# Kernel tuning notes

Measured on AMD Instinct MI355X. Metric: run time of the kernel, lower is better.

## Reference

```python
import jax, jax.numpy as jnp
import numpy as np

N_E = 512; KEY_DIM = 512; E_DIM = 512; E_SPLIT = 8
KT = 0.1; COE_EMA = 0.5; RATE = 1.2
HALF_PI = float(np.pi / 2.0)


def l2n(x, eps=1e-12):
    # torch F.normalize(p=2, dim=-1)
    return x / jnp.maximum(jnp.linalg.norm(x, axis=-1, keepdims=True), eps)


def sphere_emb(feature, t):
    # TimeSphereEncoder: lift unit feature in R^d to R^{d+1} with time angle
    # a = t * (pi/2) / rate ; out = [feature*cos(a), sin(a)]
    a = t * (HALF_PI / RATE)
    return jnp.concatenate([feature * jnp.cos(a)[..., None], jnp.sin(a)[..., None]], axis=-1)


def split_t_f(x):
    # inverse of sphere_emb for unit-norm x: recover (t, sin_component, feature)
    s = x[..., -1]
    t = jnp.arcsin(jnp.clip(s, -1.0, 1.0)) / (HALF_PI / RATE)
    f = l2n(x[..., :-1])
    return t, s, f


def split_norm(v):
    # split_vparams_norm: L2-normalize each of E_SPLIT contiguous chunks
    shp = v.shape
    d = E_DIM // E_SPLIT
    return l2n(v.reshape(shp[:-1] + (E_SPLIT, d))).reshape(shp)


def setup_inputs() -> dict:
    key = jax.random.key(0)
    k = jax.random.split(key, 6)
    key_soft = jax.random.normal(k[0], (32, 1024, KEY_DIM), jnp.float32)
    u_t = jax.random.uniform(k[1], (32, 1024), jnp.float32)
    keys_weight = l2n(jax.random.uniform(k[2], (N_E, KEY_DIM), jnp.float32, -1.0 / N_E, 1.0 / N_E))
    t_keys_weight = (jnp.arange(N_E, dtype=jnp.float32)[:, None]
                     + jax.random.uniform(k[3], (N_E, 1), jnp.float32)) / N_E
    r_keys_weight = jnp.full((N_E, 1), 0.999, jnp.float32)
    vparams_weight = jax.random.uniform(k[4], (N_E, E_DIM), jnp.float32, -1.0 / N_E, 1.0 / N_E)
    return {"key_soft": key_soft, "u_t": u_t, "keys_weight": keys_weight,
            "t_keys_weight": t_keys_weight, "r_keys_weight": r_keys_weight,
            "vparams_weight": vparams_weight}


def _forward(key_soft, u_t, keys_weight, t_keys_weight, r_keys_weight, vparams_weight):
    sg = jax.lax.stop_gradient
    B, T, D = key_soft.shape
    BT = B * T
    # normalize + time-embed tokens
    ks_emb = sphere_emb(l2n(key_soft), u_t)                       # (B,T,D+1)
    ks_flat = ks_emb.reshape(BT, D + 1)
    # codebook keys: normalized, time-embedded, detached, scaled by hardtanh(r)
    keys_norm = sphere_emb(l2n(keys_weight), t_keys_weight[:, 0])  # (n_e,D+1)
    r = jnp.clip(r_keys_weight, 0.0, 1.0)                          # (n_e,1)
    keysA = sg(keys_norm) * r
    score0 = ks_flat @ keysA.T                                     # (BT,n_e)
    idx0 = jnp.argmax(score0, axis=1)
    # --- EMA codebook update (all no-grad) ---
    ks_sg = sg(ks_flat)
    seg = jax.ops.segment_sum(ks_sg, idx0, num_segments=N_E)       # (n_e,D+1)
    cnt = jax.ops.segment_sum(jnp.ones((BT,), ks_sg.dtype), idx0, num_segments=N_E)[:, None]
    mean_ks = jnp.nan_to_num(seg / (1.0 + cnt))
    keys_new_full = l2n(sg(keysA) * COE_EMA + mean_ks * (1.0 - COE_EMA))
    t_new, _, feat_new = split_t_f(keys_new_full)
    index_switch = jnp.argsort(t_new)
    t_sorted = t_new[index_switch]
    keys_feat2 = feat_new[index_switch]
    r2 = jnp.clip(r_keys_weight[index_switch], 0.0, 1.0)
    vparams2 = vparams_weight[index_switch]
    idx1 = index_switch[idx0]
    cnt2 = jax.ops.segment_sum(jnp.ones((BT,), ks_sg.dtype), idx1, num_segments=N_E) + 1.0
    w_cnt = sg(jnp.nan_to_num(1.0 / cnt2)[idx1].reshape(B, T))
    # --- second scoring with updated codebook ---
    keys_norm2 = sphere_emb(l2n(keys_feat2), t_sorted)             # (n_e,D+1)
    keysB = sg(keys_norm2) * r2
    score = ks_flat @ keysB.T                                      # (BT,n_e)
    w = jnp.nan_to_num(jax.nn.softmax(score / KT, axis=-1))
    w_max = jnp.take_along_axis(w, idx1[:, None], axis=-1)[:, 0].reshape(B, T)
    vpn = split_norm(vparams2)
    vp_w = split_norm(w @ sg(vpn))                                 # (BT,e_dim)
    key_w = l2n(w @ sg(keysB))                                     # (BT,D+1)
    vparams_hard = split_norm(vparams2[idx1])
    key_hard_raw = keysB[idx1]
    vparams_hard = vp_w + sg(vparams_hard - vp_w)                  # straight-through
    key_hard = key_w + sg(key_hard_raw - key_w)
    return (idx1.reshape(B, T),
            key_hard.reshape(B, T, D + 1),
            vp_w.reshape(B, T, E_DIM),
            vparams_hard.reshape(B, T, E_DIM),
            w_max, w_cnt, ks_emb)


def reference(key_soft, u_t, keys_weight, t_keys_weight, r_keys_weight, vparams_weight):
    return _forward(key_soft, u_t, keys_weight, t_keys_weight, r_keys_weight, vparams_weight)
```

## Files before the change

kernel.cpp:

```cpp
#include <hip/hip_runtime.h>
#include <math.h>

constexpr int BT  = 32768;
constexpr int D   = 512;
constexpr int D1  = 513;
constexpr int NE  = 512;
constexpr int EDIM = 512;
constexpr int NCH = 128;
constexpr int SUB = 32;
constexpr int P1S = 520;
constexpr int AKP = 544;
constexpr int A16S = 2 * AKP;
#define KA 1.3089969389957472f

typedef _Float16 h16;
typedef _Float16 f16x8 __attribute__((ext_vector_type(8)));
typedef _Float16 f16x4 __attribute__((ext_vector_type(4)));
typedef float f32x4 __attribute__((ext_vector_type(4)));

__device__ __forceinline__ float wave_sum(float v) {
#pragma unroll
  for (int off = 32; off; off >>= 1) v += __shfl_xor(v, off);
  return v;
}

__global__ __launch_bounds__(256) void k_embed(const float* __restrict__ ks,
                                               const float* __restrict__ ut,
                                               float* __restrict__ emb) {
  int token = blockIdx.x * 4 + (threadIdx.x >> 6);
  int lane = threadIdx.x & 63;
  const float4* row4 = (const float4*)(ks + (size_t)token * D);
  float4 va = row4[lane * 2];
  float4 vb = row4[lane * 2 + 1];
  float ss = va.x * va.x + va.y * va.y + va.z * va.z + va.w * va.w
           + vb.x * vb.x + vb.y * vb.y + vb.z * vb.z + vb.w * vb.w;
  ss = wave_sum(ss);
  float inv = 1.0f / fmaxf(sqrtf(ss), 1e-12f);
  float a = ut[token] * KA;
  float c = cosf(a), s = sinf(a);
  float ic = inv * c;
  float* o = emb + (size_t)token * D1 + lane * 8;
  o[0] = va.x * ic; o[1] = va.y * ic; o[2] = va.z * ic; o[3] = va.w * ic;
  o[4] = vb.x * ic; o[5] = vb.y * ic; o[6] = vb.z * ic; o[7] = vb.w * ic;
  if (lane == 0) emb[(size_t)token * D1 + D] = s;
}

__global__ __launch_bounds__(64) void k_keysA(const float* __restrict__ kw,
                                              const float* __restrict__ tk,
                                              const float* __restrict__ rk,
                                              float* __restrict__ keysA,
                                              h16* __restrict__ BA) {
  int e = blockIdx.x; int lane = threadIdx.x;
  const float* row = kw + (size_t)e * D;
  float v[8]; float ss = 0.f;
#pragma unroll
  for (int i = 0; i < 8; i++) { v[i] = row[lane + 64 * i]; ss += v[i] * v[i]; }
  ss = wave_sum(ss);
  float inv = 1.0f / fmaxf(sqrtf(ss), 1e-12f);
  float a = tk[e] * KA;
  float r = fminf(fmaxf(rk[e], 0.f), 1.f);
  float c = cosf(a) * r, s = sinf(a) * r;
  float* o = keysA + (size_t)e * D1;
  h16* br = BA + (size_t)e * A16S;
#pragma unroll
  for (int i = 0; i < 8; i++) {
    float val = v[i] * inv * c;
    o[lane + 64 * i] = val;
    float x = val * 8.0f;
    h16 h = (h16)x;
    br[lane + 64 * i] = h;
    br[AKP + lane + 64 * i] = (h16)(x - (float)h);
  }
  if (lane == 0) {
    o[D] = s;
    float x = s * 8.0f;
    h16 h = (h16)x;
    br[512] = h;
    br[AKP + 512] = (h16)(x - (float)h);
  }
  if (lane >= 1 && lane < 32) {
    br[512 + lane] = (h16)0.f;
    br[AKP + 512 + lane] = (h16)0.f;
  }
}

template <int KP, int EPI, int ASRC, int TERMS>
__global__ __launch_bounds__(256) void k_gemm(const float* __restrict__ Af,
                                              const h16* __restrict__ Ai,
                                              const h16* __restrict__ Bp,
                                              float* __restrict__ C,
                                              unsigned short* __restrict__ W,
                                              float* __restrict__ pv,
                                              int* __restrict__ pi_,
                                              float* __restrict__ ps) {
  constexpr int NS = KP / 32;
  constexpr int LST = 36;
  __shared__ h16 Ah[128 * LST];
  __shared__ h16 Al[(TERMS >= 2) ? 128 * LST : 1];
  __shared__ h16 Bh[128 * LST];
  __shared__ h16 Bl[(TERMS >= 3) ? 128 * LST : 1];
  const int tid = threadIdx.x;
  const int bid = blockIdx.x;
  const int wg = (bid & 7) * (gridDim.x >> 3) + (bid >> 3);
  const int m0 = (wg >> 2) * 128;
  const int n0 = (wg & 3) * 128;
  const int nblk = wg & 3;
  const int lane = tid & 63;
  const int wid = tid >> 6;
  const int wr = wid >> 1, wc = wid & 1;
  const int l15 = lane & 15, l4 = lane >> 4;
  const int aB = (wr * 64 + l15) * LST + l4 * 8;
  const int bB = (wc * 64 + l15) * LST + l4 * 8;

  f32x4 acc[4][4] = {};

  auto loadAf = [&](int s, float fv[4][4]) {
    int k0 = s * 32;
    bool guard = (KP == AKP) && (k0 + 32 > D1);
#pragma unroll
    for (int p = 0; p < 4; ++p) {
      int row = (tid >> 3) + 32 * p;
      int fq = tid & 7;
      const float* ap = Af + (size_t)(m0 + row) * D1 + k0 + fq * 4;
      if (!guard) {
#pragma unroll
        for (int j = 0; j < 4; ++j) fv[p][j] = ap[j];
      } else {
#pragma unroll
        for (int j = 0; j < 4; ++j) {
          int c = k0 + fq * 4 + j;
          fv[p][j] = (c < D1) ? ap[j] : 0.f;
        }
      }
    }
  };
  auto writeAf = [&](float fv[4][4]) {
#pragma unroll
    for (int p = 0; p < 4; ++p) {
      int row = (tid >> 3) + 32 * p;
      int fq = tid & 7;
      f16x4 hh, ll;
#pragma unroll
      for (int j = 0; j < 4; ++j) {
        float x = fv[p][j] * 8.0f;
        h16 h = (h16)x;
        hh[j] = h;
        ll[j] = (h16)(x - (float)h);
      }
      *(f16x4*)&Ah[row * LST + fq * 4] = hh;
      if constexpr (TERMS >= 2) *(f16x4*)&Al[row * LST + fq * 4] = ll;
    }
  };
  auto loadAp = [&](int s, uint4 av[2]) {
    int k0 = s * 32;
#pragma unroll
    for (int p = 0; p < 2; ++p) {
      int lin = tid + 256 * p;
      int row = lin >> 2, q = lin & 3;
      av[p] = *(const uint4*)(Ai + (size_t)(m0 + row) * 512 + k0 + q * 8);
    }
  };
  auto writeAp = [&](uint4 av[2]) {
#pragma unroll
    for (int p = 0; p < 2; ++p) {
      int lin = tid + 256 * p;
      int row = lin >> 2, q = lin & 3;
      *(uint4*)&Ah[row * LST + q * 8] = av[p];
    }
  };
  constexpr int BPASS = (TERMS >= 3) ? 4 : 2;
  auto loadB = [&](int s, uint4 bv[BPASS]) {
    int k0 = s * 32;
#pragma unroll
    for (int p = 0; p < BPASS; ++p) {
      int lin = tid + 256 * p;
      int row = (lin >> 2) & 127;
      int half = lin >> 9;
      int q = lin & 3;
      bv[p] = *(const uint4*)(Bp + (size_t)(n0 + row) * (2 * KP) + half * KP + k0 + q * 8);
    }
  };
  auto writeB = [&](uint4 bv[BPASS]) {
#pragma unroll
    for (int p = 0; p < BPASS; ++p) {
      int lin = tid + 256 * p;
      int row = (lin >> 2) & 127;
      int half = lin >> 9;
      int q = lin & 3;
      h16* dst = (half && TERMS >= 3) ? Bl : Bh;
      *(uint4*)&dst[row * LST + q * 8] = bv[p];
    }
  };

  {
    uint4 bv[BPASS];
    loadB(0, bv);
    if constexpr (ASRC == 0) { float fv[4][4]; loadAf(0, fv); writeAf(fv); }
    else { uint4 av[2]; loadAp(0, av); writeAp(av); }
    writeB(bv);
  }
  __syncthreads();

  for (int s = 0; s < NS; ++s) {
    uint4 apn[2], bvn[BPASS]; float fvn[4][4];
    if (s + 1 < NS) {
      if constexpr (ASRC == 0) loadAf(s + 1, fvn);
      else loadAp(s + 1, apn);
      loadB(s + 1, bvn);
    }
    f16x8 ah[4], al_[4], bh_[4], bl_[4];
#pragma unroll
    for (int i = 0; i < 4; ++i) {
      ah[i] = *(const f16x8*)&Ah[aB + i * 16 * LST];
      if constexpr (TERMS >= 2) al_[i] = *(const f16x8*)&Al[aB + i * 16 * LST];
    }
#pragma unroll
    for (int j = 0; j < 4; ++j) {
      bh_[j] = *(const f16x8*)&Bh[bB + j * 16 * LST];
      if constexpr (TERMS >= 3) bl_[j] = *(const f16x8*)&Bl[bB + j * 16 * LST];
    }
    __syncthreads();
    if (s + 1 < NS) {
      if constexpr (ASRC == 0) writeAf(fvn);
      else writeAp(apn);
      writeB(bvn);
    }
#pragma unroll
    for (int j = 0; j < 4; ++j) {
#pragma unroll
      for (int i = 0; i < 4; ++i) {
        acc[i][j] = __builtin_amdgcn_mfma_f32_16x16x32_f16(ah[i], bh_[j], acc[i][j], 0, 0, 0);
        if constexpr (TERMS >= 2)
          acc[i][j] = __builtin_amdgcn_mfma_f32_16x16x32_f16(al_[i], bh_[j], acc[i][j], 0, 0, 0);
        if constexpr (TERMS >= 3)
          acc[i][j] = __builtin_amdgcn_mfma_f32_16x16x32_f16(ah[i], bl_[j], acc[i][j], 0, 0, 0);
      }
    }
    __syncthreads();
  }

  if constexpr (EPI == 1) {
#pragma unroll
    for (int i = 0; i < 4; ++i)
#pragma unroll
      for (int r = 0; r < 4; ++r) {
        float ss = 0.f;
#pragma unroll
        for (int j = 0; j < 4; ++j) ss += acc[i][j][r] * acc[i][j][r];
        ss += __shfl_xor(ss, 1); ss += __shfl_xor(ss, 2);
        ss += __shfl_xor(ss, 4); ss += __shfl_xor(ss, 8);
        float inv = 1.0f / fmaxf(sqrtf(ss), 1e-12f);
        int row = m0 + wr * 64 + i * 16 + l4 * 4 + r;
        float* cp = C + (size_t)row * 512 + n0 + wc * 64 + l15;
#pragma unroll
        for (int j = 0; j < 4; ++j) cp[j * 16] = acc[i][j][r] * inv;
      }
  } else if constexpr (EPI == 2) {
    float* lv = (float*)Ah;
    int*   li = (int*)Bh;
#pragma unroll
    for (int i = 0; i < 4; ++i)
#pragma unroll
      for (int r = 0; r < 4; ++r) {
        float bv = -INFINITY; int bidx = 0x7fffffff;
#pragma unroll
        for (int j = 0; j < 4; ++j) {
          float val = acc[i][j][r] * 0.015625f;
          int col = n0 + wc * 64 + j * 16 + l15;
          if (val > bv || (val == bv && col < bidx)) { bv = val; bidx = col; }
        }
#pragma unroll
        for (int off = 1; off < 16; off <<= 1) {
          float ov = __shfl_xor(bv, off);
          int oi = __shfl_xor(bidx, off);
          if (ov > bv || (ov == bv && oi < bidx)) { bv = ov; bidx = oi; }
        }
        if (l15 == 0) {
          int lr = wr * 64 + i * 16 + l4 * 4 + r;
          lv[wc * 128 + lr] = bv; li[wc * 128 + lr] = bidx;
        }
      }
    __syncthreads();
    if (tid < 128) {
      float v0 = lv[tid], v1 = lv[128 + tid];
      int i0 = li[tid], i1 = li[128 + tid];
      bool sec = (v1 > v0) || (v1 == v0 && i1 < i0);
      int row = m0 + tid;
      pv[(size_t)row * 4 + nblk] = sec ? v1 : v0;
      pi_[(size_t)row * 4 + nblk] = sec ? i1 : i0;
    }
  } else if constexpr (EPI == 3) {
    float* psW = (float*)Bh;
#pragma unroll
    for (int i = 0; i < 4; ++i)
#pragma unroll
      for (int r = 0; r < 4; ++r) {
        int row = m0 + wr * 64 + i * 16 + l4 * 4 + r;
        unsigned short* wp = W + (size_t)row * 512 + n0 + wc * 64 + l15;
        float se = 0.f;
#pragma unroll
        for (int j = 0; j < 4; ++j) {
          float v = acc[i][j][r] * 0.015625f;
          float w = __expf(10.f * v);
          se += w;
          h16 hh = (h16)w;
          wp[j * 16] = *(unsigned short*)&hh;
        }
        se += __shfl_xor(se, 1); se += __shfl_xor(se, 2);
        se += __shfl_xor(se, 4); se += __shfl_xor(se, 8);
        if (l15 == 0) psW[wc * 128 + wr * 64 + i * 16 + l4 * 4 + r] = se;
      }
    __syncthreads();
    if (tid < 128)
      ps[(size_t)(m0 + tid) * 4 + nblk] = psW[tid] + psW[128 + tid];
  }
}

__global__ __launch_bounds__(256) void k_hist_chunks(const float* __restrict__ pval,
                                                     const int* __restrict__ pidx,
                                                     int* __restrict__ idx0,
                                                     int* __restrict__ hist2,
                                                     int* __restrict__ myrank) {
  __shared__ int lidx[256];
  __shared__ int hist[NE];
  int tid = threadIdx.x;
  int chunk = blockIdx.x;
  int t = chunk * 256 + tid;
  float bv = pval[(size_t)t * 4];
  int bi = pidx[(size_t)t * 4];
#pragma unroll
  for (int b = 1; b < 4; ++b) {
    float v = pval[(size_t)t * 4 + b];
    if (v > bv) { bv = v; bi = pidx[(size_t)t * 4 + b]; }
  }
  idx0[t] = bi;
  lidx[tid] = bi;
  hist[tid] = 0; hist[tid + 256] = 0;
  __syncthreads();
  int j = lidx[tid];
  int rank = 0;
  for (int i = 0; i < tid; ++i) rank += (lidx[i] == j);
  myrank[t] = rank;
  atomicAdd(&hist[j], 1);
  __syncthreads();
  hist2[chunk * NE + tid] = hist[tid];
  hist2[chunk * NE + tid + 256] = hist[tid + 256];
}

__global__ __launch_bounds__(512) void k_scan(const int* __restrict__ hist2,
                                              int* __restrict__ offs,
                                              int* __restrict__ chunk_base,
                                              float* __restrict__ cntf) {
  __shared__ int sh[NE];
  int c = threadIdx.x;
  int tot = 0;
  for (int k = 0; k < NCH; ++k) tot += hist2[k * NE + c];
  cntf[c] = (float)tot;
  sh[c] = tot;
  __syncthreads();
  for (int off = 1; off < NE; off <<= 1) {
    int v = (c >= off) ? sh[c - off] : 0;
    __syncthreads();
    sh[c] += v;
    __syncthreads();
  }
  int excl = sh[c] - tot;
  offs[c] = excl;
  int run = excl;
  for (int k = 0; k < NCH; ++k) {
    chunk_base[k * NE + c] = run;
    run += hist2[k * NE + c];
  }
}

__global__ __launch_bounds__(256) void k_scatter(const int* __restrict__ idx0,
                                                 const int* __restrict__ myrank,
                                                 const int* __restrict__ chunk_base,
                                                 int* __restrict__ tok_sorted) {
  int tid = threadIdx.x;
  int chunk = blockIdx.x;
  int t = chunk * 256 + tid;
  int j = idx0[t];
  tok_sorted[chunk_base[chunk * NE + j] + myrank[t]] = t;
}

__global__ __launch_bounds__(256) void k_seg1(const int* __restrict__ tok_sorted,
                                              const int* __restrict__ offs,
                                              const float* __restrict__ cntf,
                                              const float* __restrict__ emb,
                                              float* __restrict__ part1) {
  __shared__ float part[4][512];
  __shared__ float p512[4];
  int e = blockIdx.x, sub = blockIdx.y;
  int tid = threadIdx.x;
  int wave = tid >> 6, lane = tid & 63;
  int start = offs[e];
  int n = (int)cntf[e];
  float acc[8] = {}; float a512 = 0.f;
  for (int k = sub * 4 + wave; k < n; k += SUB * 4) {
    int t = tok_sorted[start + k];
    const float* row = emb + (size_t)t * D1;
#pragma unroll
    for (int i = 0; i < 8; ++i) acc[i] += row[lane + 64 * i];
    if (lane == 0) a512 += row[512];
  }
#pragma unroll
  for (int i = 0; i < 8; ++i) part[wave][lane + 64 * i] = acc[i];
  if (lane == 0) p512[wave] = a512;
  __syncthreads();
  float* o = part1 + (size_t)(e * SUB + sub) * P1S;
  o[tid] = part[0][tid] + part[1][tid] + part[2][tid] + part[3][tid];
  o[tid + 256] = part[0][tid + 256] + part[1][tid + 256] + part[2][tid + 256] + part[3][tid + 256];
  if (tid == 0) o[512] = p512[0] + p512[1] + p512[2] + p512[3];
}

__global__ __launch_bounds__(256) void k_seg2(const float* __restrict__ part1,
                                              const float* __restrict__ cntf,
                                              const float* __restrict__ keysA,
                                              float* __restrict__ feat,
                                              float* __restrict__ tnew) {
  __shared__ float r4[4];
  __shared__ float r4b[4];
  int e = blockIdx.x;
  int tid = threadIdx.x;
  int wave = tid >> 6, lane = tid & 63;
  float s0 = 0.f, s1 = 0.f, s512 = 0.f;
  for (int sub = 0; sub < SUB; ++sub) {
    const float* p = part1 + (size_t)(e * SUB + sub) * P1S;
    s0 += p[tid]; s1 += p[tid + 256]; s512 += p[512];
  }
  float c = cntf[e];
  float rinv = 1.0f / (1.0f + c);
  float x0 = keysA[(size_t)e * D1 + tid] * 0.5f + (s0 * rinv) * 0.5f;
  float x1 = keysA[(size_t)e * D1 + tid + 256] * 0.5f + (s1 * rinv) * 0.5f;
  float x512 = keysA[(size_t)e * D1 + 512] * 0.5f + (s512 * rinv) * 0.5f;
  float ssp = x0 * x0 + x1 * x1;
  float w = wave_sum(ssp);
  if (lane == 0) r4[wave] = w;
  __syncthreads();
  float ss = r4[0] + r4[1] + r4[2] + r4[3] + x512 * x512;
  float inv = 1.0f / fmaxf(sqrtf(ss), 1e-12f);
  if (tid == 0) {
    float sc = fminf(fmaxf(x512 * inv, -1.0f), 1.0f);
    tnew[e] = asinf(sc) / KA;
  }
  float f0 = x0 * inv, f1 = x1 * inv;
  float ssp2 = f0 * f0 + f1 * f1;
  float w2 = wave_sum(ssp2);
  if (lane == 0) r4b[wave] = w2;
  __syncthreads();
  float ss2 = r4b[0] + r4b[1] + r4b[2] + r4b[3];
  float inv2 = 1.0f / fmaxf(sqrtf(ss2), 1e-12f);
  feat[(size_t)e * D + tid] = f0 * inv2;
  feat[(size_t)e * D + tid + 256] = f1 * inv2;
}

__global__ __launch_bounds__(512) void k_argsort(const float* __restrict__ tnew,
                                                 int* __restrict__ perm) {
  __shared__ float t[NE];
  int i = threadIdx.x;
  t[i] = tnew[i];
  __syncthreads();
  float ti = t[i];
  int rank = 0;
  for (int j = 0; j < NE; j++) {
    float tj = t[j];
    rank += (tj < ti) || (tj == ti && j < i);
  }
  perm[rank] = i;
}

__global__ __launch_bounds__(64) void k_build(const int* __restrict__ perm,
                                              const float* __restrict__ tnew,
                                              const float* __restrict__ rk,
                                              const float* __restrict__ feat,
                                              const float* __restrict__ vparams,
                                              float* __restrict__ keysB,
                                              h16* __restrict__ BB,
                                              float* __restrict__ vpn,
                                              h16* __restrict__ BV) {
  int p = blockIdx.x; int lane = threadIdx.x;
  int src = perm[p];
  float t = tnew[src];
  float a = t * KA;
  float r2 = fminf(fmaxf(rk[src], 0.f), 1.f);
  float f[8]; float ss = 0.f;
#pragma unroll
  for (int i = 0; i < 8; i++) { f[i] = feat[(size_t)src * D + lane + 64 * i]; ss += f[i] * f[i]; }
  ss = wave_sum(ss);
  float inv = 1.0f / fmaxf(sqrtf(ss), 1e-12f);
  float c = cosf(a) * r2, s = sinf(a) * r2;
  h16* br = BB + (size_t)p * A16S;
#pragma unroll
  for (int i = 0; i < 8; i++) {
    float val = f[i] * inv * c;
    keysB[(size_t)p * D1 + lane + 64 * i] = val;
    float x = val * 8.0f;
    h16 h = (h16)x;
    br[lane + 64 * i] = h;
    br[AKP + lane + 64 * i] = (h16)(x - (float)h);
  }
  if (lane == 0) {
    keysB[(size_t)p * D1 + D] = s;
    float x = s * 8.0f;
    h16 h = (h16)x;
    br[512] = h;
    br[AKP + 512] = (h16)(x - (float)h);
  }
  if (lane >= 1 && lane < 32) {
    br[512 + lane] = (h16)0.f;
    br[AKP + 512 + lane] = (h16)0.f;
  }
#pragma unroll
  for (int i = 0; i < 8; i++) {
    float vp = vparams[(size_t)src * EDIM + lane + 64 * i];
    float ssc = wave_sum(vp * vp);
    float invc = 1.0f / fmaxf(sqrtf(ssc), 1e-12f);
    float val = vp * invc;
    int d = lane + 64 * i;
    vpn[(size_t)p * EDIM + d] = val;
    float x = val * 8.0f;
    h16 hi = (h16)x;
    BV[(size_t)d * (2 * NE) + p] = hi;
    BV[(size_t)d * (2 * NE) + NE + p] = (h16)(x - (float)hi);
  }
}

__global__ __launch_bounds__(256) void k_gather(const int* __restrict__ idx0,
                                                const int* __restrict__ perm,
                                                const float* __restrict__ cntf,
                                                const float* __restrict__ keysB,
                                                const float* __restrict__ vpn,
                                                const float* __restrict__ ps,
                                                const unsigned short* __restrict__ W,
                                                float* __restrict__ O0,
                                                float* __restrict__ O1,
                                                float* __restrict__ O3,
                                                float* __restrict__ O4,
                                                float* __restrict__ O5) {
  int t = blockIdx.x * 4 + (threadIdx.x >> 6);
  int lane = threadIdx.x & 63;
  int i0 = idx0[t];
  int j = perm[i0];
#pragma unroll
  for (int i = 0; i < 9; i++) {
    int d = lane + 64 * i;
    if (d < D1) O1[(size_t)t * D1 + d] = keysB[(size_t)j * D1 + d];
  }
#pragma unroll
  for (int i = 0; i < 8; i++) {
    int d = lane + 64 * i;
    O3[(size_t)t * EDIM + d] = vpn[(size_t)j * EDIM + d];
  }
  if (lane == 0) {
    O0[t] = (float)j;
    O5[t] = 1.0f / (cntf[i0] + 1.0f);
    float S = ps[(size_t)t * 4] + ps[(size_t)t * 4 + 1]
            + ps[(size_t)t * 4 + 2] + ps[(size_t)t * 4 + 3];
    unsigned short u = W[(size_t)t * 512 + j];
    O4[t] = (float)(*(const h16*)&u) / S;
  }
}

extern "C" void kernel_launch(void* const* d_in, const int* in_sizes, int n_in,
                              void* d_out, int out_size, void* d_ws, size_t ws_size,
                              hipStream_t stream) {
  const float* key_soft = (const float*)d_in[0];
  const float* u_t      = (const float*)d_in[1];
  const float* keys_w   = (const float*)d_in[2];
  const float* t_keys   = (const float*)d_in[3];
  const float* r_keys   = (const float*)d_in[4];
  const float* vparams  = (const float*)d_in[5];

  float* out = (float*)d_out;
  float* O0 = out;
  float* O1 = O0 + (size_t)BT;
  float* O2 = O1 + (size_t)BT * D1;
  float* O3 = O2 + (size_t)BT * EDIM;
  float* O4 = O3 + (size_t)BT * EDIM;
  float* O5 = O4 + (size_t)BT;
  float* O6 = O5 + (size_t)BT;

  float* ws = (float*)d_ws;
  size_t off = 0;
  auto alloc = [&](size_t n) { float* p = ws + off; off += (n + 63) & ~(size_t)63; return p; };
  unsigned short* w16 = (unsigned short*)alloc((size_t)BT * 256);
  float* part1  = alloc((size_t)NE * SUB * P1S);
  float* keysA  = alloc((size_t)NE * D1);
  float* keysB  = alloc((size_t)NE * D1);
  float* feat   = alloc((size_t)NE * D);
  float* vpn    = alloc((size_t)NE * EDIM);
  float* tnew   = alloc(NE);
  float* cntf   = alloc(NE);
  h16*   BA     = (h16*)alloc((size_t)NE * AKP);
  h16*   BB     = (h16*)alloc((size_t)NE * AKP);
  h16*   BV     = (h16*)alloc((size_t)EDIM * NE);
  float* pval   = alloc((size_t)BT * 4);
  int*   pidx   = (int*)alloc((size_t)BT * 4);
  float* ps2    = alloc((size_t)BT * 4);
  int*   idx0   = (int*)alloc(BT);
  int*   perm   = (int*)alloc(NE);
  int*   myrank = (int*)alloc(BT);
  int*   tok_sorted = (int*)alloc(BT);
  int*   hist2  = (int*)alloc((size_t)NCH * NE);
  int*   chunk_base = (int*)alloc((size_t)NCH * NE);
  int*   offsb  = (int*)alloc(NE);

  k_embed<<<BT / 4, 256, 0, stream>>>(key_soft, u_t, O6);
  k_keysA<<<NE, 64, 0, stream>>>(keys_w, t_keys, r_keys, keysA, BA);
  k_gemm<AKP, 2, 0, 3><<<1024, 256, 0, stream>>>(O6, nullptr, BA,
                                                 nullptr, nullptr, pval, pidx, nullptr);
  k_hist_chunks<<<NCH, 256, 0, stream>>>(pval, pidx, idx0, hist2, myrank);
  k_scan<<<1, NE, 0, stream>>>(hist2, offsb, chunk_base, cntf);
  k_scatter<<<NCH, 256, 0, stream>>>(idx0, myrank, chunk_base, tok_sorted);
  k_seg1<<<dim3(NE, SUB), 256, 0, stream>>>(tok_sorted, offsb, cntf, O6, part1);
  k_seg2<<<NE, 256, 0, stream>>>(part1, cntf, keysA, feat, tnew);
  k_argsort<<<1, NE, 0, stream>>>(tnew, perm);
  k_build<<<NE, 64, 0, stream>>>(perm, tnew, r_keys, feat, vparams, keysB, BB, vpn, BV);
  k_gemm<AKP, 3, 0, 2><<<1024, 256, 0, stream>>>(O6, nullptr, BB,
                                                 nullptr, w16, nullptr, nullptr, ps2);
  k_gemm<512, 1, 2, 1><<<1024, 256, 0, stream>>>(nullptr, (const h16*)w16, BV,
                                                 O2, nullptr, nullptr, nullptr, nullptr);
  k_gather<<<BT / 4, 256, 0, stream>>>(idx0, perm, cntf, keysB, vpn, ps2, w16,
                                       O0, O1, O3, O4, O5);
}
```

Measured before the change: 419.1 us.

## Fold token normalization and time embedding into GEMM A-operand loads

Per-token scale (inv-norm times cos) and sine values are now computed by a small norms kernel. Both scoring GEMMs read the raw key_soft rows with aligned float4 loads and apply the scale on the fly, instead of reading the stride-513 embedded buffer. The embedded output is still written afterwards for the returned result, but it no longer sits before the GEMMs. This replaces unaligned scalar loads with vector loads and removes the embed kernel from the GEMM dependency chain, at the cost of reading key_soft one extra time.

After: 433.0 us. 1.03x slower.

```diff
diff --git a/kernel.cpp b/kernel.cpp
--- a/kernel.cpp
+++ b/kernel.cpp
@@ -24,9 +24,10 @@
   return v;
 }
 
-__global__ __launch_bounds__(256) void k_embed(const float* __restrict__ ks,
+__global__ __launch_bounds__(256) void k_norms(const float* __restrict__ ks,
                                                const float* __restrict__ ut,
-                                               float* __restrict__ emb) {
+                                               float* __restrict__ icv,
+                                               float* __restrict__ sinv) {
   int token = blockIdx.x * 4 + (threadIdx.x >> 6);
   int lane = threadIdx.x & 63;
   const float4* row4 = (const float4*)(ks + (size_t)token * D);
@@ -35,14 +36,28 @@
   float ss = va.x * va.x + va.y * va.y + va.z * va.z + va.w * va.w
            + vb.x * vb.x + vb.y * vb.y + vb.z * vb.z + vb.w * vb.w;
   ss = wave_sum(ss);
-  float inv = 1.0f / fmaxf(sqrtf(ss), 1e-12f);
-  float a = ut[token] * KA;
-  float c = cosf(a), s = sinf(a);
-  float ic = inv * c;
+  if (lane == 0) {
+    float inv = 1.0f / fmaxf(sqrtf(ss), 1e-12f);
+    float a = ut[token] * KA;
+    icv[token] = inv * cosf(a);
+    sinv[token] = sinf(a);
+  }
+}
+
+__global__ __launch_bounds__(256) void k_embed(const float* __restrict__ ks,
+                                               const float* __restrict__ icv,
+                                               const float* __restrict__ sinv,
+                                               float* __restrict__ emb) {
+  int token = blockIdx.x * 4 + (threadIdx.x >> 6);
+  int lane = threadIdx.x & 63;
+  const float4* row4 = (const float4*)(ks + (size_t)token * D);
+  float4 va = row4[lane * 2];
+  float4 vb = row4[lane * 2 + 1];
+  float ic = icv[token];
   float* o = emb + (size_t)token * D1 + lane * 8;
   o[0] = va.x * ic; o[1] = va.y * ic; o[2] = va.z * ic; o[3] = va.w * ic;
   o[4] = vb.x * ic; o[5] = vb.y * ic; o[6] = vb.z * ic; o[7] = vb.w * ic;
-  if (lane == 0) emb[(size_t)token * D1 + D] = s;
+  if (lane == 0) emb[(size_t)token * D1 + D] = sinv[token];
 }
 
 __global__ __launch_bounds__(64) void k_keysA(const float* __restrict__ kw,
@@ -86,6 +101,8 @@
 
 template <int KP, int EPI, int ASRC, int TERMS>
 __global__ __launch_bounds__(256) void k_gemm(const float* __restrict__ Af,
+                                              const float* __restrict__ icv,
+                                              const float* __restrict__ sinv,
                                               const h16* __restrict__ Ai,
                                               const h16* __restrict__ Bp,
                                               float* __restrict__ C,
@@ -114,22 +131,32 @@
 
   f32x4 acc[4][4] = {};
 
+  float ic4[4], sv4[4];
+  if constexpr (ASRC == 0) {
+#pragma unroll
+    for (int p = 0; p < 4; ++p) {
+      int row = m0 + (tid >> 3) + 32 * p;
+      ic4[p] = icv[row];
+      sv4[p] = sinv[row];
+    }
+  }
+
   auto loadAf = [&](int s, float fv[4][4]) {
     int k0 = s * 32;
-    bool guard = (KP == AKP) && (k0 + 32 > D1);
+    bool guard = (KP == AKP) && (k0 + 32 > D);
 #pragma unroll
     for (int p = 0; p < 4; ++p) {
       int row = (tid >> 3) + 32 * p;
       int fq = tid & 7;
-      const float* ap = Af + (size_t)(m0 + row) * D1 + k0 + fq * 4;
       if (!guard) {
-#pragma unroll
-        for (int j = 0; j < 4; ++j) fv[p][j] = ap[j];
+        float4 v = *(const float4*)(Af + (size_t)(m0 + row) * D + k0 + fq * 4);
+        fv[p][0] = v.x * ic4[p]; fv[p][1] = v.y * ic4[p];
+        fv[p][2] = v.z * ic4[p]; fv[p][3] = v.w * ic4[p];
       } else {
 #pragma unroll
         for (int j = 0; j < 4; ++j) {
           int c = k0 + fq * 4 + j;
-          fv[p][j] = (c < D1) ? ap[j] : 0.f;
+          fv[p][j] = (c == D) ? sv4[p] : 0.f;
         }
       }
     }
@@ -595,6 +622,8 @@
   h16*   BA     = (h16*)alloc((size_t)NE * AKP);
   h16*   BB     = (h16*)alloc((size_t)NE * AKP);
   h16*   BV     = (h16*)alloc((size_t)EDIM * NE);
+  float* icv    = alloc(BT);
+  float* sinv   = alloc(BT);
   float* pval   = alloc((size_t)BT * 4);
   int*   pidx   = (int*)alloc((size_t)BT * 4);
   float* ps2    = alloc((size_t)BT * 4);
@@ -606,10 +635,11 @@
   int*   chunk_base = (int*)alloc((size_t)NCH * NE);
   int*   offsb  = (int*)alloc(NE);
 
-  k_embed<<<BT / 4, 256, 0, stream>>>(key_soft, u_t, O6);
+  k_norms<<<BT / 4, 256, 0, stream>>>(key_soft, u_t, icv, sinv);
   k_keysA<<<NE, 64, 0, stream>>>(keys_w, t_keys, r_keys, keysA, BA);
-  k_gemm<AKP, 2, 0, 3><<<1024, 256, 0, stream>>>(O6, nullptr, BA,
+  k_gemm<AKP, 2, 0, 3><<<1024, 256, 0, stream>>>(key_soft, icv, sinv, nullptr, BA,
                                                  nullptr, nullptr, pval, pidx, nullptr);
+  k_embed<<<BT / 4, 256, 0, stream>>>(key_soft, icv, sinv, O6);
   k_hist_chunks<<<NCH, 256, 0, stream>>>(pval, pidx, idx0, hist2, myrank);
   k_scan<<<1, NE, 0, stream>>>(hist2, offsb, chunk_base, cntf);
   k_scatter<<<NCH, 256, 0, stream>>>(idx0, myrank, chunk_base, tok_sorted);
@@ -617,9 +647,10 @@
   k_seg2<<<NE, 256, 0, stream>>>(part1, cntf, keysA, feat, tnew);
   k_argsort<<<1, NE, 0, stream>>>(tnew, perm);
   k_build<<<NE, 64, 0, stream>>>(perm, tnew, r_keys, feat, vparams, keysB, BB, vpn, BV);
-  k_gemm<AKP, 3, 0, 2><<<1024, 256, 0, stream>>>(O6, nullptr, BB,
+  k_gemm<AKP, 3, 0, 2><<<1024, 256, 0, stream>>>(key_soft, icv, sinv, nullptr, BB,
                                                  nullptr, w16, nullptr, nullptr, ps2);
-  k_gemm<512, 1, 2, 1><<<1024, 256, 0, stream>>>(nullptr, (const h16*)w16, BV,
+  k_gemm<512, 1, 2, 1><<<1024, 256, 0, stream>>>(nullptr, nullptr, nullptr,
+                                                 (const h16*)w16, BV,
                                                  O2, nullptr, nullptr, nullptr, nullptr);
   k_gather<<<BT / 4, 256, 0, stream>>>(idx0, perm, cntf, keysB, vpn, ps2, w16,
                                        O0, O1, O3, O4, O5);
```
